# Kernel optimization log

Hardware: AMD Instinct MI355X
Metric: run time of the kernel (lower is better)

## Reference

```python
import jax, jax.numpy as jnp
import numpy as np

DIM = 128
NH = 4          # num_heads
NFQ = 4         # num_frames_q
NFKV = 2        # num_frames_kv
WH, WW = 8, 8   # window size
BW = 1024       # B * nW
NW = 64         # number of windows per image


def _rel_index():
    # Faithful port of the torch buffer construction (meshgrid indexing='ij').
    cdq = np.arange(NFQ)
    cdkv = np.arange(0, NFQ, (NFQ + 1) // NFKV)
    ch = np.arange(WH)
    cw = np.arange(WW)
    cq = np.stack(np.meshgrid(cdq, ch, cw, indexing='ij')).reshape(3, -1)
    ckv = np.stack(np.meshgrid(cdkv, ch, cw, indexing='ij')).reshape(3, -1)
    rel = (cq[:, :, None] - ckv[:, None, :]).transpose(1, 2, 0).astype(np.int64)
    rel[:, :, 0] += NFQ - 1
    rel[:, :, 1] += WH - 1
    rel[:, :, 2] += WW - 1
    rel[:, :, 0] *= (2 * WH - 1) * (2 * WW - 1)
    rel[:, :, 1] *= 2 * WW - 1
    return jnp.asarray(rel.sum(-1), dtype=jnp.int32)  # (N1, N2)


def setup_inputs() -> dict:
    key = jax.random.key(0)
    ks = jax.random.split(key, 8)
    N1 = NFQ * WH * WW
    N2 = NFKV * WH * WW
    L = (2 * NFQ - 1) * (2 * WH - 1) * (2 * WW - 1)
    return {
        "q": jax.random.normal(ks[0], (BW, N1, DIM), jnp.float32),
        "kv": jax.random.normal(ks[1], (BW, N2, DIM), jnp.float32),
        "mask": jax.random.normal(ks[2], (NW, N1, N2), jnp.float32),
        "q_w": jax.random.normal(ks[3], (DIM, DIM), jnp.float32) * 0.02,
        "q_b": jnp.zeros((DIM,), jnp.float32),
        "kv_w": jax.random.normal(ks[4], (2 * DIM, DIM), jnp.float32) * 0.02,
        "kv_b": jnp.zeros((2 * DIM,), jnp.float32),
        "proj_w": jax.random.normal(ks[5], (DIM, DIM), jnp.float32) * 0.02,
        "proj_b": jnp.zeros((DIM,), jnp.float32),
        "rpb_table": jax.random.normal(ks[6], (L, NH), jnp.float32) * 0.02,
        "rel_index": _rel_index(),
    }


def reference(q, kv, mask, q_w, q_b, kv_w, kv_b, proj_w, proj_b, rpb_table, rel_index):
    B_, N1, C = q.shape
    N2 = kv.shape[1]
    hd = C // NH
    scale = hd ** (-0.5)
    # projections (torch Linear: x @ W.T + b)
    qh = (q @ q_w.T + q_b).reshape(B_, N1, NH, hd).transpose(0, 2, 1, 3) * scale  # (B_,H,N1,hd)
    kvh = (kv @ kv_w.T + kv_b).reshape(B_, N2, 2, NH, hd).transpose(2, 0, 3, 1, 4)
    k, v = kvh[0], kvh[1]  # (B_,H,N2,hd)
    attn = jnp.einsum('bhqd,bhkd->bhqk', qh, k)  # (B_,H,N1,N2)
    bias = rpb_table[rel_index].transpose(2, 0, 1)  # (H,N1,N2)
    attn = attn + bias[None]
    nW = mask.shape[0]
    attn = attn.reshape(B_ // nW, nW, NH, N1, N2) + mask[None, :, None]
    attn = jax.nn.softmax(attn.reshape(B_, NH, N1, N2), axis=-1)
    x = jnp.einsum('bhqk,bhkd->bqhd', attn, v).reshape(B_, N1, C)
    x = x @ proj_w.T + proj_b
    return (x, attn)
```

## Files before the change

kernel.cpp:

```cpp
#include <hip/hip_runtime.h>


typedef __attribute__((ext_vector_type(8))) short s16x8;
typedef __attribute__((ext_vector_type(4))) short s16x4;
typedef __attribute__((ext_vector_type(4))) float f32x4;

static __device__ __forceinline__ unsigned short f2bf(float f) {
  union { float f; unsigned u; } v; v.f = f;
  unsigned r = v.u + 0x7FFFu + ((v.u >> 16) & 1u);
  return (unsigned short)(r >> 16);
}

static __device__ __forceinline__ s16x8 cvt8(f32x4 a0, f32x4 a1) {
  s16x8 r;
  r[0] = (short)f2bf(a0[0]); r[1] = (short)f2bf(a0[1]);
  r[2] = (short)f2bf(a0[2]); r[3] = (short)f2bf(a0[3]);
  r[4] = (short)f2bf(a1[0]); r[5] = (short)f2bf(a1[1]);
  r[6] = (short)f2bf(a1[2]); r[7] = (short)f2bf(a1[3]);
  return r;
}

__global__ void kw_prep(const float* __restrict__ qw, const float* __restrict__ kvw,
                        const float* __restrict__ pw, const float* __restrict__ rpb,
                        const int* __restrict__ relidx, const float* __restrict__ mask,
                        unsigned short* __restrict__ qwb, unsigned short* __restrict__ kvwb,
                        unsigned short* __restrict__ pwb, float* __restrict__ bm) {
  int tid = blockIdx.x * 256 + threadIdx.x;
  int stride = gridDim.x * 256;
  for (int i = tid; i < 65536; i += stride) {
    if (i < 16384)      qwb[i] = f2bf(qw[i]);
    else if (i < 49152) kvwb[i - 16384] = f2bf(kvw[i - 16384]);
    else                pwb[i - 49152] = f2bf(pw[i - 49152]);
  }
  for (int i = tid; i < 2097152; i += stride) {
    int wdw = i >> 15, j = i & 32767;
    int rel = relidx[j];
    float4 tv = *(const float4*)(rpb + rel * 4);
    float mk = mask[i];
    float* d = bm + (size_t)(wdw * 4) * 32768 + j;
    d[0]      = tv.x + mk;
    d[32768]  = tv.y + mk;
    d[65536]  = tv.z + mk;
    d[98304]  = tv.w + mk;
  }
}

__global__ __launch_bounds__(256) void kkv(const float* __restrict__ kv,
    const unsigned short* __restrict__ kvwb, const float* __restrict__ kvb,
    unsigned short* __restrict__ kws, unsigned short* __restrict__ vT) {
  __shared__ unsigned short oK[64][136];
  __shared__ unsigned short oV[128][72];
  int b = blockIdx.x >> 1, r0 = (blockIdx.x & 1) << 6;
  int t = threadIdx.x;
  int w = t >> 6, l = t & 63, lm = l & 15, lg = l >> 4;
  const float* arow = kv + (size_t)(b * 128 + r0 + w * 16 + lm) * 128;
  f32x4 acc[16];
#pragma unroll
  for (int i = 0; i < 16; ++i) acc[i] = (f32x4){0.f, 0.f, 0.f, 0.f};
#pragma unroll
  for (int kk = 0; kk < 4; ++kk) {
    f32x4 a0 = __builtin_nontemporal_load((const f32x4*)(arow + kk * 32 + lg * 8));
    f32x4 a1 = __builtin_nontemporal_load((const f32x4*)(arow + kk * 32 + lg * 8 + 4));
    s16x8 a = cvt8(a0, a1);
#pragma unroll
    for (int ct = 0; ct < 16; ++ct) {
      s16x8 bf = *(const s16x8*)(kvwb + (ct * 16 + lm) * 128 + kk * 32 + lg * 8);
      acc[ct] = __builtin_amdgcn_mfma_f32_16x16x32_bf16(a, bf, acc[ct], 0, 0, 0);
    }
  }
#pragma unroll
  for (int ct = 0; ct < 16; ++ct) {
    int col = ct * 16 + lm;
    float bb = kvb[col];
    if (col < 128) {
#pragma unroll
      for (int r = 0; r < 4; ++r)
        oK[w * 16 + lg * 4 + r][col] = f2bf(acc[ct][r] + bb);
    } else {
      int d = col - 128;
      s16x4 pk;
#pragma unroll
      for (int r = 0; r < 4; ++r) pk[r] = (short)f2bf(acc[ct][r] + bb);
      *(s16x4*)&oV[d][w * 16 + lg * 4] = pk;
    }
  }
  __syncthreads();
  {
    int o = t * 8, row = o >> 5, cs = o & 31;
#pragma unroll
    for (int h = 0; h < 4; ++h) {
      s16x8 v = *(const s16x8*)&oK[row][h * 32 + cs];
      *(s16x8*)(kws + ((size_t)(b * 4 + h) * 128 + r0 + row) * 32 + cs) = v;
    }
  }
#pragma unroll
  for (int i = 0; i < 4; ++i) {
    int o = (t + i * 256) * 8;
    int d = o >> 6, ns = o & 63;
    s16x8 v = *(const s16x8*)&oV[d][ns];
    *(s16x8*)(vT + ((size_t)b * 128 + d) * 128 + r0 + ns) = v;
  }
}

__global__ __launch_bounds__(256, 3) void kfused(const float* __restrict__ q,
    const unsigned short* __restrict__ qwb, const float* __restrict__ qb,
    const unsigned short* __restrict__ kws, const unsigned short* __restrict__ vT,
    const float* __restrict__ bm, const unsigned short* __restrict__ pwb,
    const float* __restrict__ pb, float* __restrict__ attn_out,
    float* __restrict__ xout) {
  __shared__ unsigned short qhL[64][136];
  __shared__ unsigned short XL[64][136];
  __shared__ float scratch[4][1088] __attribute__((aligned(16)));
  int bid = blockIdx.x;
  int wdw = bid >> 6, r = bid & 63;
  int b = wdw + (r >> 2) * 64;
  int q0 = (r & 3) << 6;
  int t = threadIdx.x;
  int w = t >> 6, l = t & 63, lm = l & 15, lg = l >> 4;
  float* aSt = scratch[w];
  const f32x4 zero = {0.f, 0.f, 0.f, 0.f};

  {
    const float* arow = q + (size_t)(b * 256 + q0 + w * 16 + lm) * 128;
    f32x4 acc[8];
#pragma unroll
    for (int i = 0; i < 8; ++i) acc[i] = zero;
#pragma unroll
    for (int kk = 0; kk < 4; ++kk) {
      f32x4 a0 = __builtin_nontemporal_load((const f32x4*)(arow + kk * 32 + lg * 8));
      f32x4 a1 = __builtin_nontemporal_load((const f32x4*)(arow + kk * 32 + lg * 8 + 4));
      s16x8 a = cvt8(a0, a1);
#pragma unroll
      for (int ct = 0; ct < 8; ++ct) {
        s16x8 bf = *(const s16x8*)(qwb + (ct * 16 + lm) * 128 + kk * 32 + lg * 8);
        acc[ct] = __builtin_amdgcn_mfma_f32_16x16x32_bf16(a, bf, acc[ct], 0, 0, 0);
      }
    }
    const float SC = 0.17677669529663687f;
#pragma unroll
    for (int ct = 0; ct < 8; ++ct) {
      int col = ct * 16 + lm;
      float bb = qb[col];
#pragma unroll
      for (int r2 = 0; r2 < 4; ++r2)
        qhL[w * 16 + lg * 4 + r2][col] = f2bf((acc[ct][r2] + bb) * SC);
    }
  }
  __syncthreads();

  {
    int h = w;
    const unsigned short* ksrc = kws + (size_t)(b * 4 + h) * 4096;
    const unsigned short* vsrc = vT + (size_t)(b * 4 + h) * 4096;
    const float* bmh = bm + (size_t)(wdw * 4 + h) * 32768;
    float* attnh = attn_out + ((size_t)(b * 4 + h) * 256 + q0) * 128;
    for (int qt = 0; qt < 4; ++qt) {
      int qg = q0 + qt * 16 + lm;
      s16x8 bq = *(const s16x8*)&qhL[qt * 16 + lm][h * 32 + lg * 8];
      f32x4 S[8];
#pragma unroll
      for (int ct = 0; ct < 8; ++ct) {
        s16x8 ak = *(const s16x8*)(ksrc + (ct * 16 + lm) * 32 + lg * 8);
        S[ct] = __builtin_amdgcn_mfma_f32_16x16x32_bf16(ak, bq, zero, 0, 0, 0);
      }
      float m = -1e30f;
#pragma unroll
      for (int ct = 0; ct < 8; ++ct) {
        float4 bv = *(const float4*)(bmh + (size_t)qg * 128 + ct * 16 + lg * 4);
        S[ct][0] += bv.x; S[ct][1] += bv.y; S[ct][2] += bv.z; S[ct][3] += bv.w;
        m = fmaxf(m, fmaxf(fmaxf(S[ct][0], S[ct][1]), fmaxf(S[ct][2], S[ct][3])));
      }
      m = fmaxf(m, __shfl_xor(m, 16));
      m = fmaxf(m, __shfl_xor(m, 32));
      float s = 0.f;
#pragma unroll
      for (int ct = 0; ct < 8; ++ct) {
#pragma unroll
        for (int r2 = 0; r2 < 4; ++r2) { S[ct][r2] = __expf(S[ct][r2] - m); s += S[ct][r2]; }
      }
      s += __shfl_xor(s, 16);
      s += __shfl_xor(s, 32);
      float inv = 1.0f / s;
      float* adst = attnh + qt * 16 * 128;
      s16x8 pfrag[4];
#pragma unroll
      for (int half = 0; half < 2; ++half) {
#pragma unroll
        for (int c = 0; c < 4; ++c) {
          int ct = half * 4 + c;
          f32x4 pv = { S[ct][0] * inv, S[ct][1] * inv, S[ct][2] * inv, S[ct][3] * inv };
          *(f32x4*)(aSt + lm * 68 + c * 16 + lg * 4) = pv;
        }
#pragma unroll
        for (int i = 0; i < 4; ++i) {
          int o = l * 4 + i * 256;
          int row = o >> 6, col = o & 63;
          f32x4 v = *(const f32x4*)(aSt + row * 68 + col);
          __builtin_nontemporal_store(v, (f32x4*)(adst + row * 128 + half * 64 + col));
        }
#pragma unroll
        for (int k2 = 0; k2 < 2; ++k2) {
          const float* pp = aSt + lm * 68 + k2 * 32 + lg * 8;
          pfrag[half * 2 + k2] = cvt8(*(const f32x4*)pp, *(const f32x4*)(pp + 4));
        }
      }
      f32x4 O[2];
      O[0] = zero; O[1] = zero;
#pragma unroll
      for (int kk = 0; kk < 4; ++kk) {
#pragma unroll
        for (int cd = 0; cd < 2; ++cd) {
          s16x8 av = *(const s16x8*)(vsrc + (cd * 16 + lm) * 128 + kk * 32 + lg * 8);
          O[cd] = __builtin_amdgcn_mfma_f32_16x16x32_bf16(av, pfrag[kk], O[cd], 0, 0, 0);
        }
      }
#pragma unroll
      for (int cd = 0; cd < 2; ++cd) {
        s16x4 pk;
#pragma unroll
        for (int r2 = 0; r2 < 4; ++r2) pk[r2] = (short)f2bf(O[cd][r2]);
        *(s16x4*)&XL[qt * 16 + lm][h * 32 + cd * 16 + lg * 4] = pk;
      }
    }
  }
  __syncthreads();

  {
    f32x4 acc[8];
#pragma unroll
    for (int i = 0; i < 8; ++i) acc[i] = zero;
#pragma unroll
    for (int kk = 0; kk < 4; ++kk) {
      s16x8 a = *(const s16x8*)&XL[w * 16 + lm][kk * 32 + lg * 8];
#pragma unroll
      for (int ct = 0; ct < 8; ++ct) {
        s16x8 bf = *(const s16x8*)(pwb + (ct * 16 + lm) * 128 + kk * 32 + lg * 8);
        acc[ct] = __builtin_amdgcn_mfma_f32_16x16x32_bf16(a, bf, acc[ct], 0, 0, 0);
      }
    }
#pragma unroll
    for (int ct = 0; ct < 8; ++ct) {
      int col = ct * 16 + lm;
      float bb = pb[col];
#pragma unroll
      for (int r2 = 0; r2 < 4; ++r2) acc[ct][r2] += bb;
    }
    float* xdst = xout + ((size_t)b * 256 + q0 + w * 16) * 128;
#pragma unroll
    for (int half = 0; half < 2; ++half) {
#pragma unroll
      for (int c = 0; c < 4; ++c) {
        int ct = half * 4 + c;
#pragma unroll
        for (int r2 = 0; r2 < 4; ++r2)
          aSt[(lg * 4 + r2) * 68 + c * 16 + lm] = acc[ct][r2];
      }
#pragma unroll
      for (int i = 0; i < 4; ++i) {
        int o = l * 4 + i * 256;
        int row = o >> 6, col = o & 63;
        f32x4 v = *(const f32x4*)(aSt + row * 68 + col);
        __builtin_nontemporal_store(v, (f32x4*)(xdst + row * 128 + half * 64 + col));
      }
    }
  }
}

extern "C" void kernel_launch(void* const* d_in, const int* in_sizes, int n_in,
                              void* d_out, int out_size, void* d_ws, size_t ws_size,
                              hipStream_t stream) {
  const float* q    = (const float*)d_in[0];
  const float* kv   = (const float*)d_in[1];
  const float* mask = (const float*)d_in[2];
  const float* qw   = (const float*)d_in[3];
  const float* qb   = (const float*)d_in[4];
  const float* kvw  = (const float*)d_in[5];
  const float* kvb  = (const float*)d_in[6];
  const float* pw   = (const float*)d_in[7];
  const float* pb   = (const float*)d_in[8];
  const float* rpb  = (const float*)d_in[9];
  const int* relidx = (const int*)d_in[10];

  float* xout = (float*)d_out;
  float* attn = xout + (size_t)1024 * 256 * 128;

  char* ws = (char*)d_ws;
  unsigned short* qwb  = (unsigned short*)ws;
  unsigned short* kvwb = (unsigned short*)(ws + 32768);
  unsigned short* pwb  = (unsigned short*)(ws + 98304);
  float*          bm   = (float*)(ws + 131072);
  unsigned short* kws  = (unsigned short*)(ws + 131072 + 33554432);
  unsigned short* vT   = kws + (size_t)16777216;

  kw_prep<<<2048, 256, 0, stream>>>(qw, kvw, pw, rpb, relidx, mask, qwb, kvwb, pwb, bm);
  kkv<<<2048, 256, 0, stream>>>(kv, kvwb, kvb, kws, vT);
  kfused<<<4096, 256, 0, stream>>>(q, qwb, qb, kws, vT, bm, pwb, pb, attn, xout);
}
```

Baseline: 413.3 us.

## Stop materializing combined bias+mask; add bias and mask inside fused kernel

The prep kernel no longer builds a 32 MB per-window, per-head bias+mask tensor. It builds only a small per-head relative bias table, and the fused kernel reads bias and mask separately and adds them. This removes a large write and re-read of global memory. The change also remaps block indices so that blocks sharing a window and its mask run close together, and hoists the V fragment loads ahead of the QK MFMAs to hide latency, at the cost of more registers.

```diff
diff --git a/kernel.cpp b/kernel.cpp
--- a/kernel.cpp
+++ b/kernel.cpp
@@ -22,9 +22,9 @@
 
 __global__ void kw_prep(const float* __restrict__ qw, const float* __restrict__ kvw,
                         const float* __restrict__ pw, const float* __restrict__ rpb,
-                        const int* __restrict__ relidx, const float* __restrict__ mask,
+                        const int* __restrict__ relidx,
                         unsigned short* __restrict__ qwb, unsigned short* __restrict__ kvwb,
-                        unsigned short* __restrict__ pwb, float* __restrict__ bm) {
+                        unsigned short* __restrict__ pwb, float* __restrict__ biasT) {
   int tid = blockIdx.x * 256 + threadIdx.x;
   int stride = gridDim.x * 256;
   for (int i = tid; i < 65536; i += stride) {
@@ -32,16 +32,13 @@
     else if (i < 49152) kvwb[i - 16384] = f2bf(kvw[i - 16384]);
     else                pwb[i - 49152] = f2bf(pw[i - 49152]);
   }
-  for (int i = tid; i < 2097152; i += stride) {
-    int wdw = i >> 15, j = i & 32767;
-    int rel = relidx[j];
-    float4 tv = *(const float4*)(rpb + rel * 4);
-    float mk = mask[i];
-    float* d = bm + (size_t)(wdw * 4) * 32768 + j;
-    d[0]      = tv.x + mk;
-    d[32768]  = tv.y + mk;
-    d[65536]  = tv.z + mk;
-    d[98304]  = tv.w + mk;
+  for (int i = tid; i < 32768; i += stride) {
+    int rel = relidx[i];
+    float4 t = *(const float4*)(rpb + rel * 4);
+    biasT[i]          = t.x;
+    biasT[32768 + i]  = t.y;
+    biasT[65536 + i]  = t.z;
+    biasT[98304 + i]  = t.w;
   }
 }
 
@@ -105,16 +102,17 @@
 __global__ __launch_bounds__(256, 3) void kfused(const float* __restrict__ q,
     const unsigned short* __restrict__ qwb, const float* __restrict__ qb,
     const unsigned short* __restrict__ kws, const unsigned short* __restrict__ vT,
-    const float* __restrict__ bm, const unsigned short* __restrict__ pwb,
-    const float* __restrict__ pb, float* __restrict__ attn_out,
-    float* __restrict__ xout) {
+    const float* __restrict__ biasT, const float* __restrict__ mask,
+    const unsigned short* __restrict__ pwb, const float* __restrict__ pb,
+    float* __restrict__ attn_out, float* __restrict__ xout) {
   __shared__ unsigned short qhL[64][136];
   __shared__ unsigned short XL[64][136];
   __shared__ float scratch[4][1088] __attribute__((aligned(16)));
   int bid = blockIdx.x;
-  int wdw = bid >> 6, r = bid & 63;
-  int b = wdw + (r >> 2) * 64;
-  int q0 = (r & 3) << 6;
+  int c = bid & 7, j = (bid >> 3) & 15, hi = bid >> 7;
+  int g = hi * 8 + c;
+  int wdw = g >> 2, q0 = (g & 3) << 6;
+  int b = wdw + 64 * j;
   int t = threadIdx.x;
   int w = t >> 6, l = t & 63, lm = l & 15, lg = l >> 4;
   float* aSt = scratch[w];
@@ -152,10 +150,17 @@
     int h = w;
     const unsigned short* ksrc = kws + (size_t)(b * 4 + h) * 4096;
     const unsigned short* vsrc = vT + (size_t)(b * 4 + h) * 4096;
-    const float* bmh = bm + (size_t)(wdw * 4 + h) * 32768;
+    const float* biash = biasT + (size_t)h * 32768;
+    const float* maskw = mask + (size_t)wdw * 32768;
     float* attnh = attn_out + ((size_t)(b * 4 + h) * 256 + q0) * 128;
     for (int qt = 0; qt < 4; ++qt) {
       int qg = q0 + qt * 16 + lm;
+      s16x8 av[8];
+#pragma unroll
+      for (int kk = 0; kk < 4; ++kk)
+#pragma unroll
+        for (int cd = 0; cd < 2; ++cd)
+          av[kk * 2 + cd] = *(const s16x8*)(vsrc + (cd * 16 + lm) * 128 + kk * 32 + lg * 8);
       s16x8 bq = *(const s16x8*)&qhL[qt * 16 + lm][h * 32 + lg * 8];
       f32x4 S[8];
 #pragma unroll
@@ -166,8 +171,10 @@
       float m = -1e30f;
 #pragma unroll
       for (int ct = 0; ct < 8; ++ct) {
-        float4 bv = *(const float4*)(bmh + (size_t)qg * 128 + ct * 16 + lg * 4);
-        S[ct][0] += bv.x; S[ct][1] += bv.y; S[ct][2] += bv.z; S[ct][3] += bv.w;
+        float4 bv = *(const float4*)(biash + (size_t)qg * 128 + ct * 16 + lg * 4);
+        float4 mv = *(const float4*)(maskw + (size_t)qg * 128 + ct * 16 + lg * 4);
+        S[ct][0] += bv.x + mv.x; S[ct][1] += bv.y + mv.y;
+        S[ct][2] += bv.z + mv.z; S[ct][3] += bv.w + mv.w;
         m = fmaxf(m, fmaxf(fmaxf(S[ct][0], S[ct][1]), fmaxf(S[ct][2], S[ct][3])));
       }
       m = fmaxf(m, __shfl_xor(m, 16));
@@ -186,10 +193,10 @@
 #pragma unroll
       for (int half = 0; half < 2; ++half) {
 #pragma unroll
-        for (int c = 0; c < 4; ++c) {
-          int ct = half * 4 + c;
+        for (int cc = 0; cc < 4; ++cc) {
+          int ct = half * 4 + cc;
           f32x4 pv = { S[ct][0] * inv, S[ct][1] * inv, S[ct][2] * inv, S[ct][3] * inv };
-          *(f32x4*)(aSt + lm * 68 + c * 16 + lg * 4) = pv;
+          *(f32x4*)(aSt + lm * 68 + cc * 16 + lg * 4) = pv;
         }
 #pragma unroll
         for (int i = 0; i < 4; ++i) {
@@ -207,13 +214,10 @@
       f32x4 O[2];
       O[0] = zero; O[1] = zero;
 #pragma unroll
-      for (int kk = 0; kk < 4; ++kk) {
-#pragma unroll
-        for (int cd = 0; cd < 2; ++cd) {
-          s16x8 av = *(const s16x8*)(vsrc + (cd * 16 + lm) * 128 + kk * 32 + lg * 8);
-          O[cd] = __builtin_amdgcn_mfma_f32_16x16x32_bf16(av, pfrag[kk], O[cd], 0, 0, 0);
-        }
-      }
+      for (int kk = 0; kk < 4; ++kk)
+#pragma unroll
+        for (int cd = 0; cd < 2; ++cd)
+          O[cd] = __builtin_amdgcn_mfma_f32_16x16x32_bf16(av[kk * 2 + cd], pfrag[kk], O[cd], 0, 0, 0);
 #pragma unroll
       for (int cd = 0; cd < 2; ++cd) {
         s16x4 pk;
@@ -249,11 +253,11 @@
 #pragma unroll
     for (int half = 0; half < 2; ++half) {
 #pragma unroll
-      for (int c = 0; c < 4; ++c) {
-        int ct = half * 4 + c;
+      for (int cc = 0; cc < 4; ++cc) {
+        int ct = half * 4 + cc;
 #pragma unroll
         for (int r2 = 0; r2 < 4; ++r2)
-          aSt[(lg * 4 + r2) * 68 + c * 16 + lm] = acc[ct][r2];
+          aSt[(lg * 4 + r2) * 68 + cc * 16 + lm] = acc[ct][r2];
       }
 #pragma unroll
       for (int i = 0; i < 4; ++i) {
@@ -285,14 +289,14 @@
   float* attn = xout + (size_t)1024 * 256 * 128;
 
   char* ws = (char*)d_ws;
-  unsigned short* qwb  = (unsigned short*)ws;
-  unsigned short* kvwb = (unsigned short*)(ws + 32768);
-  unsigned short* pwb  = (unsigned short*)(ws + 98304);
-  float*          bm   = (float*)(ws + 131072);
-  unsigned short* kws  = (unsigned short*)(ws + 131072 + 33554432);
-  unsigned short* vT   = kws + (size_t)16777216;
-
-  kw_prep<<<2048, 256, 0, stream>>>(qw, kvw, pw, rpb, relidx, mask, qwb, kvwb, pwb, bm);
+  unsigned short* qwb   = (unsigned short*)ws;
+  unsigned short* kvwb  = (unsigned short*)(ws + 32768);
+  unsigned short* pwb   = (unsigned short*)(ws + 98304);
+  float*          biasT = (float*)(ws + 131072);
+  unsigned short* kws   = (unsigned short*)(ws + 655360);
+  unsigned short* vT    = kws + (size_t)16777216;
+
+  kw_prep<<<256, 256, 0, stream>>>(qw, kvw, pw, rpb, relidx, qwb, kvwb, pwb, biasT);
   kkv<<<2048, 256, 0, stream>>>(kv, kvwb, kvb, kws, vT);
-  kfused<<<4096, 256, 0, stream>>>(q, qwb, qb, kws, vT, bm, pwb, pb, attn, xout);
-}
+  kfused<<<4096, 256, 0, stream>>>(q, qwb, qb, kws, vT, biasT, mask, pwb, pb, attn, xout);
+}
```

Result: slower. 440.3 us (+6.5%).

## Hoist K/V fragments to registers and software-pipeline bias+mask loads

Applied to the files above, without the earlier changes.

Loads the per-head K and V MFMA fragments into registers once per block instead of reloading them for every query tile. Prefetches the next tile's bias+mask values into a double-buffered register set while the current tile computes. Double-buffers the per-wave LDS staging area and replaces __syncthreads with a bare LDS waitcnt plus s_barrier. The extra register use forces lowering launch bounds from 3 to 2 blocks per SM, which trades occupancy for latency hiding.

```diff
diff --git a/kernel.cpp b/kernel.cpp
--- a/kernel.cpp
+++ b/kernel.cpp
@@ -102,7 +102,7 @@
   }
 }
 
-__global__ __launch_bounds__(256, 3) void kfused(const float* __restrict__ q,
+__global__ __launch_bounds__(256, 2) void kfused(const float* __restrict__ q,
     const unsigned short* __restrict__ qwb, const float* __restrict__ qb,
     const unsigned short* __restrict__ kws, const unsigned short* __restrict__ vT,
     const float* __restrict__ bm, const unsigned short* __restrict__ pwb,
@@ -110,14 +110,13 @@
     float* __restrict__ xout) {
   __shared__ unsigned short qhL[64][136];
   __shared__ unsigned short XL[64][136];
-  __shared__ float scratch[4][1088] __attribute__((aligned(16)));
+  __shared__ float scratch[4][2176] __attribute__((aligned(16)));
   int bid = blockIdx.x;
-  int wdw = bid >> 6, r = bid & 63;
-  int b = wdw + (r >> 2) * 64;
-  int q0 = (r & 3) << 6;
+  int wdw = bid >> 6, rr = bid & 63;
+  int b = wdw + (rr >> 2) * 64;
+  int q0 = (rr & 3) << 6;
   int t = threadIdx.x;
   int w = t >> 6, l = t & 63, lm = l & 15, lg = l >> 4;
-  float* aSt = scratch[w];
   const f32x4 zero = {0.f, 0.f, 0.f, 0.f};
 
   {
@@ -146,28 +145,49 @@
         qhL[w * 16 + lg * 4 + r2][col] = f2bf((acc[ct][r2] + bb) * SC);
     }
   }
-  __syncthreads();
+  asm volatile("s_waitcnt lgkmcnt(0)" ::: "memory");
+  __builtin_amdgcn_s_barrier();
 
   {
     int h = w;
     const unsigned short* ksrc = kws + (size_t)(b * 4 + h) * 4096;
     const unsigned short* vsrc = vT + (size_t)(b * 4 + h) * 4096;
-    const float* bmh = bm + (size_t)(wdw * 4 + h) * 32768;
+    const float* bmh = bm + ((size_t)(wdw * 4 + h) * 256 + q0) * 128;
     float* attnh = attn_out + ((size_t)(b * 4 + h) * 256 + q0) * 128;
-    for (int qt = 0; qt < 4; ++qt) {
-      int qg = q0 + qt * 16 + lm;
+    float* aSt0 = scratch[w];
+    float* aSt1 = scratch[w] + 1088;
+
+    s16x8 ak[8], av[8];
+#pragma unroll
+    for (int ct = 0; ct < 8; ++ct)
+      ak[ct] = *(const s16x8*)(ksrc + (ct * 16 + lm) * 32 + lg * 8);
+#pragma unroll
+    for (int kk = 0; kk < 4; ++kk)
+#pragma unroll
+      for (int cd = 0; cd < 2; ++cd)
+        av[kk * 2 + cd] = *(const s16x8*)(vsrc + (cd * 16 + lm) * 128 + kk * 32 + lg * 8);
+
+    f32x4 bmA[8], bmB[8];
+#pragma unroll
+    for (int ct = 0; ct < 8; ++ct)
+      bmA[ct] = *(const f32x4*)(bmh + (size_t)lm * 128 + ct * 16 + lg * 4);
+
+    auto body = [&](int qt, f32x4* bmc, f32x4* bmn, bool pre) {
+      if (pre) {
+#pragma unroll
+        for (int ct = 0; ct < 8; ++ct)
+          bmn[ct] = *(const f32x4*)(bmh + (size_t)((qt + 1) * 16 + lm) * 128 + ct * 16 + lg * 4);
+      }
       s16x8 bq = *(const s16x8*)&qhL[qt * 16 + lm][h * 32 + lg * 8];
       f32x4 S[8];
 #pragma unroll
+      for (int ct = 0; ct < 8; ++ct)
+        S[ct] = __builtin_amdgcn_mfma_f32_16x16x32_bf16(ak[ct], bq, zero, 0, 0, 0);
+      float m = -1e30f;
+#pragma unroll
       for (int ct = 0; ct < 8; ++ct) {
-        s16x8 ak = *(const s16x8*)(ksrc + (ct * 16 + lm) * 32 + lg * 8);
-        S[ct] = __builtin_amdgcn_mfma_f32_16x16x32_bf16(ak, bq, zero, 0, 0, 0);
-      }
-      float m = -1e30f;
-#pragma unroll
-      for (int ct = 0; ct < 8; ++ct) {
-        float4 bv = *(const float4*)(bmh + (size_t)qg * 128 + ct * 16 + lg * 4);
-        S[ct][0] += bv.x; S[ct][1] += bv.y; S[ct][2] += bv.z; S[ct][3] += bv.w;
+        S[ct][0] += bmc[ct][0]; S[ct][1] += bmc[ct][1];
+        S[ct][2] += bmc[ct][2]; S[ct][3] += bmc[ct][3];
         m = fmaxf(m, fmaxf(fmaxf(S[ct][0], S[ct][1]), fmaxf(S[ct][2], S[ct][3])));
       }
       m = fmaxf(m, __shfl_xor(m, 16));
@@ -185,35 +205,33 @@
       s16x8 pfrag[4];
 #pragma unroll
       for (int half = 0; half < 2; ++half) {
-#pragma unroll
-        for (int c = 0; c < 4; ++c) {
-          int ct = half * 4 + c;
+        float* A = half ? aSt1 : aSt0;
+#pragma unroll
+        for (int cc = 0; cc < 4; ++cc) {
+          int ct = half * 4 + cc;
           f32x4 pv = { S[ct][0] * inv, S[ct][1] * inv, S[ct][2] * inv, S[ct][3] * inv };
-          *(f32x4*)(aSt + lm * 68 + c * 16 + lg * 4) = pv;
+          *(f32x4*)(A + lm * 68 + cc * 16 + lg * 4) = pv;
         }
 #pragma unroll
         for (int i = 0; i < 4; ++i) {
           int o = l * 4 + i * 256;
           int row = o >> 6, col = o & 63;
-          f32x4 v = *(const f32x4*)(aSt + row * 68 + col);
+          f32x4 v = *(const f32x4*)(A + row * 68 + col);
           __builtin_nontemporal_store(v, (f32x4*)(adst + row * 128 + half * 64 + col));
         }
 #pragma unroll
         for (int k2 = 0; k2 < 2; ++k2) {
-          const float* pp = aSt + lm * 68 + k2 * 32 + lg * 8;
+          const float* pp = A + lm * 68 + k2 * 32 + lg * 8;
           pfrag[half * 2 + k2] = cvt8(*(const f32x4*)pp, *(const f32x4*)(pp + 4));
         }
       }
       f32x4 O[2];
       O[0] = zero; O[1] = zero;
 #pragma unroll
-      for (int kk = 0; kk < 4; ++kk) {
-#pragma unroll
-        for (int cd = 0; cd < 2; ++cd) {
-          s16x8 av = *(const s16x8*)(vsrc + (cd * 16 + lm) * 128 + kk * 32 + lg * 8);
-          O[cd] = __builtin_amdgcn_mfma_f32_16x16x32_bf16(av, pfrag[kk], O[cd], 0, 0, 0);
-        }
-      }
+      for (int kk = 0; kk < 4; ++kk)
+#pragma unroll
+        for (int cd = 0; cd < 2; ++cd)
+          O[cd] = __builtin_amdgcn_mfma_f32_16x16x32_bf16(av[kk * 2 + cd], pfrag[kk], O[cd], 0, 0, 0);
 #pragma unroll
       for (int cd = 0; cd < 2; ++cd) {
         s16x4 pk;
@@ -221,11 +239,17 @@
         for (int r2 = 0; r2 < 4; ++r2) pk[r2] = (short)f2bf(O[cd][r2]);
         *(s16x4*)&XL[qt * 16 + lm][h * 32 + cd * 16 + lg * 4] = pk;
       }
-    }
-  }
-  __syncthreads();
+    };
+    body(0, bmA, bmB, true);
+    body(1, bmB, bmA, true);
+    body(2, bmA, bmB, true);
+    body(3, bmB, bmA, false);
+  }
+  asm volatile("s_waitcnt lgkmcnt(0)" ::: "memory");
+  __builtin_amdgcn_s_barrier();
 
   {
+    float* aSt = scratch[w];
     f32x4 acc[8];
 #pragma unroll
     for (int i = 0; i < 8; ++i) acc[i] = zero;
@@ -248,18 +272,19 @@
     float* xdst = xout + ((size_t)b * 256 + q0 + w * 16) * 128;
 #pragma unroll
     for (int half = 0; half < 2; ++half) {
-#pragma unroll
-      for (int c = 0; c < 4; ++c) {
-        int ct = half * 4 + c;
+      float* A = half ? (scratch[w] + 1088) : aSt;
+#pragma unroll
+      for (int cc = 0; cc < 4; ++cc) {
+        int ct = half * 4 + cc;
 #pragma unroll
         for (int r2 = 0; r2 < 4; ++r2)
-          aSt[(lg * 4 + r2) * 68 + c * 16 + lm] = acc[ct][r2];
+          A[(lg * 4 + r2) * 68 + cc * 16 + lm] = acc[ct][r2];
       }
 #pragma unroll
       for (int i = 0; i < 4; ++i) {
         int o = l * 4 + i * 256;
         int row = o >> 6, col = o & 63;
-        f32x4 v = *(const f32x4*)(aSt + row * 68 + col);
+        f32x4 v = *(const f32x4*)(A + row * 68 + col);
         __builtin_nontemporal_store(v, (f32x4*)(xdst + row * 128 + half * 64 + col));
       }
     }
```

Result: no change. 418.9 us (+1.4%).
